# Performance work log

Hardware: AMD Instinct MI355X
Metric: run time of the kernel (lower is better)

## Reference

```python
import jax, jax.numpy as jnp
import numpy as np

D_DIM = 100000  # vocabulary size
W_DIM = 128     # embedding width
BATCH = 4096    # number of (center, context) index pairs


def setup_inputs() -> dict:
    key = jax.random.key(0)
    k1, k2, kw1, kb1, kw2, kb2 = jax.random.split(key, 6)
    idx1 = jax.random.randint(k1, (BATCH,), 0, D_DIM, dtype=jnp.int64 if jax.config.jax_enable_x64 else jnp.int32)
    idx2 = jax.random.randint(k2, (BATCH,), 0, D_DIM, dtype=jnp.int64 if jax.config.jax_enable_x64 else jnp.int32)
    # torch.nn.Linear(D, W): weight [W, D], bias [W], uniform(-1/sqrt(D), 1/sqrt(D))
    bound = 1.0 / np.sqrt(D_DIM)
    W1 = jax.random.uniform(kw1, (W_DIM, D_DIM), jnp.float32, -bound, bound)
    b1 = jax.random.uniform(kb1, (W_DIM,), jnp.float32, -bound, bound)
    W2 = jax.random.uniform(kw2, (W_DIM, D_DIM), jnp.float32, -bound, bound)
    b2 = jax.random.uniform(kb2, (W_DIM,), jnp.float32, -bound, bound)
    return {"idx1": idx1, "idx2": idx2, "W1": W1, "b1": b1, "W2": W2, "b2": b2}


def reference(idx1, idx2, W1, b1, W2, b2):
    # Linear(one_hot(idx)) == weight[:, idx] + bias  -> direct row (column) gather.
    p1 = W1[:, idx1].T + b1              # [B, W_dim]
    p2 = W2[:, idx2].T + b2              # [B, W_dim]
    s = jax.nn.sigmoid(jnp.sum(p1 * p2, axis=-1))  # [B]
    # original: cat([1 - sigmoid, sigmoid]) -> [B, 2]
    return jnp.stack([1.0 - s, s], axis=-1)
```

## Files before the change

### kernel.cpp

```cpp
#include <hip/hip_runtime.h>
#include <math.h>

#define D_DIM 100000
#define W_DIM 128
#define BATCH 4096
#define BPAD  7168

__global__ __launch_bounds__(1024) void bucket_sort(
    const int* __restrict__ idx1, const int* __restrict__ idx2,
    unsigned int* __restrict__ packed)
{
    __shared__ int cnt[BPAD];
    __shared__ int ranks[BATCH];
    __shared__ int wsum[16];

    const int m = blockIdx.x;
    const int* __restrict__ idx = m ? idx2 : idx1;
    const int t    = threadIdx.x;
    const int lane = t & 63;
    const int wv   = t >> 6;

    for (int i = t; i < BPAD; i += 1024) cnt[i] = 0;
    __syncthreads();

    #pragma unroll
    for (int j = 0; j < 4; ++j) {
        const int i = t + j * 1024;
        ranks[i] = atomicAdd(&cnt[idx[i] >> 4], 1);
    }
    __syncthreads();

    const int base = t * 7;
    int c[7]; int s = 0;
    #pragma unroll
    for (int j = 0; j < 7; ++j) { c[j] = cnt[base + j]; s += c[j]; }

    int inc = s;
    #pragma unroll
    for (int off = 1; off < 64; off <<= 1) {
        const int v = __shfl_up(inc, off, 64);
        if (lane >= off) inc += v;
    }
    if (lane == 63) wsum[wv] = inc;
    __syncthreads();

    if (t < 16) {
        const int v = wsum[t];
        int winc = v;
        #pragma unroll
        for (int off = 1; off < 16; off <<= 1) {
            const int u = __shfl_up(winc, off, 16);
            if (t >= off) winc += u;
        }
        wsum[t] = winc - v;
    }
    __syncthreads();

    int excl = wsum[wv] + (inc - s);
    #pragma unroll
    for (int j = 0; j < 7; ++j) { cnt[base + j] = excl; excl += c[j]; }
    __syncthreads();

    #pragma unroll
    for (int j = 0; j < 4; ++j) {
        const int i = t + j * 1024;
        const int v = idx[i];
        packed[(m << 12) + cnt[v >> 4] + ranks[i]] =
            ((unsigned)v << 12) | (unsigned)i;
    }
}

__global__ __launch_bounds__(256) void gather(
    const unsigned int* __restrict__ packed,
    const float* __restrict__ W1, const float* __restrict__ b1,
    const float* __restrict__ W2, const float* __restrict__ b2,
    float* __restrict__ P)
{
    const int bid = blockIdx.x;
    const int xcd = bid & 7;
    const int seq = bid >> 3;
    const int wv  = threadIdx.x >> 6;
    const int l   = threadIdx.x & 63;

    const int e0 = (xcd << 10) + (seq << 3) + (wv << 1);
    const int m  = e0 >> 12;

    const float* __restrict__ W  = m ? W2 : W1;
    const float* __restrict__ bb = m ? b2 : b1;

    const unsigned pk0 = packed[e0];
    const unsigned pk1 = packed[e0 + 1];
    const int b0 = pk0 & 4095; const int i0 = (int)(pk0 >> 12);
    const int b1v = pk1 & 4095; const int i1 = (int)(pk1 >> 12);

    const float* colA = W + (size_t)l * D_DIM;
    const float* colB = W + (size_t)(l + 64) * D_DIM;
    const float a0 = colA[i0];
    const float a1 = colA[i1];
    const float a2 = colB[i0];
    const float a3 = colB[i1];

    const float biasA = bb[l];
    const float biasB = bb[l + 64];

    float* dst0 = P + (((size_t)(m << 12) + b0)  << 7);
    float* dst1 = P + (((size_t)(m << 12) + b1v) << 7);
    dst0[l]      = a0 + biasA;
    dst0[l + 64] = a2 + biasB;
    dst1[l]      = a1 + biasA;
    dst1[l + 64] = a3 + biasB;
}

__global__ __launch_bounds__(256) void dot_sig(
    const float* __restrict__ P, float* __restrict__ out)
{
    const int b = (blockIdx.x << 2) + (threadIdx.x >> 6);
    const int l = threadIdx.x & 63;

    const float2 x = ((const float2*)(P + ((size_t)b << 7)))[l];
    const float2 y = ((const float2*)(P + ((size_t)(BATCH + b) << 7)))[l];
    float v = x.x * y.x + x.y * y.y;

    #pragma unroll
    for (int off = 32; off > 0; off >>= 1)
        v += __shfl_down(v, off, 64);

    if (l == 0) {
        const float s = 1.0f / (1.0f + expf(-v));
        ((float2*)out)[b] = make_float2(1.0f - s, s);
    }
}

extern "C" void kernel_launch(void* const* d_in, const int* in_sizes, int n_in,
                              void* d_out, int out_size, void* d_ws, size_t ws_size,
                              hipStream_t stream)
{
    const int*   idx1 = (const int*)  d_in[0];
    const int*   idx2 = (const int*)  d_in[1];
    const float* W1   = (const float*)d_in[2];
    const float* b1   = (const float*)d_in[3];
    const float* W2   = (const float*)d_in[4];
    const float* b2   = (const float*)d_in[5];
    float* out = (float*)d_out;

    unsigned int* packed = (unsigned int*)d_ws;
    float* P = (float*)((char*)d_ws + 32768);

    bucket_sort<<<2, 1024, 0, stream>>>(idx1, idx2, packed);
    gather<<<1024, 256, 0, stream>>>(packed, W1, b1, W2, b2, P);
    dot_sig<<<BATCH / 4, 256, 0, stream>>>(P, out);
}
```

Before: 131.7 us.

## Gather by weight row over sorted indices, store transposed, dot via inverse permutation

The gather now gives each wave one weight row and a run of 128 sorted indices, so each wave reads within a single row, and it writes results into a transposed [W_DIM][BATCH] buffer in sorted order. The sort also emits an inverse-permutation array, and the dot kernel looks up each batch element's sorted position to compute the dot product with per-thread accumulation and a shared-memory reduction across 4 waves. The goal is fewer scattered DRAM sectors in the gather, since sorted indices that land close together in one row share cache lines. In exchange, the dot kernel's reads become strided and scattered across the transposed buffer, and the XCD-aware block mapping is dropped.

```diff
diff --git a/kernel.cpp b/kernel.cpp
--- a/kernel.cpp
+++ b/kernel.cpp
@@ -8,7 +8,7 @@
 
 __global__ __launch_bounds__(1024) void bucket_sort(
     const int* __restrict__ idx1, const int* __restrict__ idx2,
-    unsigned int* __restrict__ packed)
+    int* __restrict__ sidx, int* __restrict__ inv)
 {
     __shared__ int cnt[BPAD];
     __shared__ int ranks[BATCH];
@@ -65,67 +65,62 @@
     for (int j = 0; j < 4; ++j) {
         const int i = t + j * 1024;
         const int v = idx[i];
-        packed[(m << 12) + cnt[v >> 4] + ranks[i]] =
-            ((unsigned)v << 12) | (unsigned)i;
+        const int pos = cnt[v >> 4] + ranks[i];
+        sidx[(m << 12) + pos] = v;
+        inv [(m << 12) + i]   = pos;
     }
 }
 
 __global__ __launch_bounds__(256) void gather(
-    const unsigned int* __restrict__ packed,
+    const int* __restrict__ sidx,
     const float* __restrict__ W1, const float* __restrict__ b1,
     const float* __restrict__ W2, const float* __restrict__ b2,
-    float* __restrict__ P)
+    float* __restrict__ Ps)
 {
-    const int bid = blockIdx.x;
-    const int xcd = bid & 7;
-    const int seq = bid >> 3;
-    const int wv  = threadIdx.x >> 6;
-    const int l   = threadIdx.x & 63;
+    const int g  = (blockIdx.x << 2) + (threadIdx.x >> 6);
+    const int l  = threadIdx.x & 63;
+    const int m  = g >> 12;
+    const int rem = g & 4095;
+    const int w   = rem >> 5;
+    const int p0  = ((rem & 31) << 7) + (l << 1);
 
-    const int e0 = (xcd << 10) + (seq << 3) + (wv << 1);
-    const int m  = e0 >> 12;
+    const int2 ii = *(const int2*)&sidx[(m << 12) + p0];
 
-    const float* __restrict__ W  = m ? W2 : W1;
-    const float* __restrict__ bb = m ? b2 : b1;
+    const float* __restrict__ row = (m ? W2 : W1) + (size_t)w * D_DIM;
+    const float bias = m ? b2[w] : b1[w];
 
-    const unsigned pk0 = packed[e0];
-    const unsigned pk1 = packed[e0 + 1];
-    const int b0 = pk0 & 4095; const int i0 = (int)(pk0 >> 12);
-    const int b1v = pk1 & 4095; const int i1 = (int)(pk1 >> 12);
+    const float v0 = row[ii.x] + bias;
+    const float v1 = row[ii.y] + bias;
 
-    const float* colA = W + (size_t)l * D_DIM;
-    const float* colB = W + (size_t)(l + 64) * D_DIM;
-    const float a0 = colA[i0];
-    const float a1 = colA[i1];
-    const float a2 = colB[i0];
-    const float a3 = colB[i1];
-
-    const float biasA = bb[l];
-    const float biasB = bb[l + 64];
-
-    float* dst0 = P + (((size_t)(m << 12) + b0)  << 7);
-    float* dst1 = P + (((size_t)(m << 12) + b1v) << 7);
-    dst0[l]      = a0 + biasA;
-    dst0[l + 64] = a2 + biasB;
-    dst1[l]      = a1 + biasA;
-    dst1[l + 64] = a3 + biasB;
+    float2* dst = (float2*)&Ps[(((size_t)(m << 7) + w) << 12) + p0];
+    *dst = make_float2(v0, v1);
 }
 
 __global__ __launch_bounds__(256) void dot_sig(
-    const float* __restrict__ P, float* __restrict__ out)
+    const float* __restrict__ Ps, const int* __restrict__ inv,
+    float* __restrict__ out)
 {
-    const int b = (blockIdx.x << 2) + (threadIdx.x >> 6);
-    const int l = threadIdx.x & 63;
+    __shared__ float red[4][64];
+    const int wv = threadIdx.x >> 6;
+    const int l  = threadIdx.x & 63;
+    const int b  = (blockIdx.x << 6) + l;
 
-    const float2 x = ((const float2*)(P + ((size_t)b << 7)))[l];
-    const float2 y = ((const float2*)(P + ((size_t)(BATCH + b) << 7)))[l];
-    float v = x.x * y.x + x.y * y.y;
+    const int p1 = inv[b];
+    const int p2 = inv[BATCH + b];
+    const float* __restrict__ P1 = Ps;
+    const float* __restrict__ P2 = Ps + ((size_t)W_DIM << 12);
 
+    float acc = 0.0f;
     #pragma unroll
-    for (int off = 32; off > 0; off >>= 1)
-        v += __shfl_down(v, off, 64);
+    for (int k = 0; k < 32; ++k) {
+        const int w = (wv << 5) + k;
+        acc += P1[((size_t)w << 12) + p1] * P2[((size_t)w << 12) + p2];
+    }
+    red[wv][l] = acc;
+    __syncthreads();
 
-    if (l == 0) {
+    if (wv == 0) {
+        const float v = red[0][l] + red[1][l] + red[2][l] + red[3][l];
         const float s = 1.0f / (1.0f + expf(-v));
         ((float2*)out)[b] = make_float2(1.0f - s, s);
     }
@@ -143,10 +138,11 @@
     const float* b2   = (const float*)d_in[5];
     float* out = (float*)d_out;
 
-    unsigned int* packed = (unsigned int*)d_ws;
-    float* P = (float*)((char*)d_ws + 32768);
+    int* sidx = (int*)d_ws;
+    int* inv  = sidx + 2 * BATCH;
+    float* Ps = (float*)((char*)d_ws + 65536);
 
-    bucket_sort<<<2, 1024, 0, stream>>>(idx1, idx2, packed);
-    gather<<<1024, 256, 0, stream>>>(packed, W1, b1, W2, b2, P);
-    dot_sig<<<BATCH / 4, 256, 0, stream>>>(P, out);
+    bucket_sort<<<2, 1024, 0, stream>>>(idx1, idx2, sidx, inv);
+    gather<<<2048, 256, 0, stream>>>(sidx, W1, b1, W2, b2, Ps);
+    dot_sig<<<BATCH / 64, 256, 0, stream>>>(Ps, inv, out);
 }
```

Measured after the change: 145.5 us. +10.5%, slower.
